# Kernel optimization log

Hardware: AMD Instinct MI355X
Metric: run time of the kernel (lower is better)

The kernel has to match this reference:

```python
import jax, jax.numpy as jnp
import numpy as np
import math

D_MODEL = 1024
N_HEADS = 16
HEAD_DIM = D_MODEL // N_HEADS  # 64
KV_DIM = 4 * HEAD_DIM          # 256
THETA = 10000.0
B, T = 2, 2048


def setup_inputs() -> dict:
    key = jax.random.key(0)
    ks = jax.random.split(key, 14)
    s = lambda k, *sh: jax.random.normal(k, sh, dtype=jnp.float32) * 0.02
    inp = {
        "x": jax.random.normal(ks[0], (B, T, D_MODEL), dtype=jnp.float32),
        "mask": jnp.tril(jnp.ones((T, T), dtype=jnp.int32))[None, None],  # causal [1,1,T,T]
        "Wq": s(ks[1], D_MODEL, D_MODEL), "bq": jnp.zeros((D_MODEL,), jnp.float32),
        "Wkv": s(ks[2], D_MODEL, KV_DIM), "bkv": jnp.zeros((KV_DIM,), jnp.float32),
        "Wk": s(ks[3], KV_DIM, D_MODEL), "bk": jnp.zeros((D_MODEL,), jnp.float32),
        "Wv": s(ks[4], KV_DIM, D_MODEL), "bv": jnp.zeros((D_MODEL,), jnp.float32),
        "Wo": s(ks[5], D_MODEL, D_MODEL), "bo": jnp.zeros((D_MODEL,), jnp.float32),
        "Wkr": s(ks[6], HEAD_DIM, HEAD_DIM),  # decoupled k_rope linear, no bias
    }
    return inp


def _rotate_half(x):
    x1, x2 = jnp.split(x, 2, axis=-1)
    return jnp.concatenate((-x2, x1), axis=-1)


def reference(x, mask, Wq, bq, Wkv, bkv, Wk, bk, Wv, bv, Wo, bo, Wkr):
    Bq, Tq, C = x.shape
    kv = x @ Wkv + bkv                                # [B,T,KV_DIM]
    k = (kv @ Wk + bk).reshape(Bq, Tq, N_HEADS, HEAD_DIM).transpose(0, 2, 1, 3)
    v = (kv @ Wv + bv).reshape(Bq, Tq, N_HEADS, HEAD_DIM).transpose(0, 2, 1, 3)
    q = (x @ Wq + bq).reshape(Bq, Tq, N_HEADS, HEAD_DIM).transpose(0, 2, 1, 3)

    # standard RoPE on q
    inv_freq = 1.0 / (THETA ** (jnp.arange(0, HEAD_DIM, 2, dtype=jnp.float32) / HEAD_DIM))
    t = jnp.arange(Tq, dtype=jnp.float32)
    freqs = t[:, None] * inv_freq[None, :]            # [T, D/2]
    emb = jnp.concatenate((freqs, freqs), axis=-1)    # [T, D]
    q = q * jnp.cos(emb) + _rotate_half(q) * jnp.sin(emb)

    # decoupled position path for k: scale by position index, then linear
    k = (k * t[None, None, :, None]) @ Wkr            # [B,H,T,D]

    attn = jnp.einsum('bhtd,bhsd->bhts', q, k) * (1.0 / math.sqrt(HEAD_DIM))
    attn = jnp.where(mask == 0, -jnp.inf, attn)
    attn = jax.nn.softmax(attn, axis=-1)
    y = jnp.einsum('bhts,bhsd->bhtd', attn, v)
    y = y.transpose(0, 2, 1, 3).reshape(Bq, Tq, C)
    return y @ Wo + bo
```

## Files before the change

kernel.cpp:

```cpp
#include <hip/hip_runtime.h>
#include <hip/hip_bf16.h>
#include <math.h>

typedef __bf16 bf16x8 __attribute__((ext_vector_type(8)));
typedef __bf16 bf16x4 __attribute__((ext_vector_type(4)));
typedef float  f32x4  __attribute__((ext_vector_type(4)));

#define T_SEQ 2048
#define NH    16
#define HD    64
#define DM    1024
#define QSCALE 0.18033688011112043f

__device__ __forceinline__ f32x4 mfma16(bf16x8 a, bf16x8 b, f32x4 c) {
    return __builtin_amdgcn_mfma_f32_16x16x32_bf16(a, b, c, 0, 0, 0);
}

__device__ __forceinline__ void gl2lds(const void* g, void* l) {
    __builtin_amdgcn_global_load_lds(
        (const __attribute__((address_space(1))) void*)g,
        (__attribute__((address_space(3))) void*)l, 16, 0, 0);
}

__device__ __forceinline__ void tsplit_body(const float* __restrict__ in,
                                            __bf16* __restrict__ oh, __bf16* __restrict__ ol,
                                            int K, int N, int n0, int k0, int SPLIT,
                                            float* tile )
{
    const int tid = threadIdx.x;
#pragma unroll
    for (int it = 0; it < 2; ++it) {
        int r = it * 32 + (tid >> 3), c8 = (tid & 7) * 8;
        f32x4 a0 = *(const f32x4*)&in[(size_t)(k0 + r) * N + n0 + c8];
        f32x4 a1 = *(const f32x4*)&in[(size_t)(k0 + r) * N + n0 + c8 + 4];
#pragma unroll
        for (int j = 0; j < 4; ++j) { tile[r * 65 + c8 + j] = a0[j]; tile[r * 65 + c8 + 4 + j] = a1[j]; }
    }
    __syncthreads();
    const int n = tid >> 2, kb = (tid & 3) * 16;
    bf16x8 h0, h1, l0, l1;
#pragma unroll
    for (int j = 0; j < 8; ++j) {
        float v0 = tile[(kb + j) * 65 + n], v1 = tile[(kb + 8 + j) * 65 + n];
        __bf16 hb0 = (__bf16)v0, hb1 = (__bf16)v1;
        h0[j] = hb0; h1[j] = hb1;
        if (SPLIT) { l0[j] = (__bf16)(v0 - (float)hb0); l1[j] = (__bf16)(v1 - (float)hb1); }
    }
    size_t o = (size_t)(n0 + n) * K + k0 + kb;
    *(bf16x8*)&oh[o] = h0; *(bf16x8*)&oh[o + 8] = h1;
    if (SPLIT) { *(bf16x8*)&ol[o] = l0; *(bf16x8*)&ol[o + 8] = l1; }
}

__global__ __launch_bounds__(256)
void prep(const float* __restrict__ x, const float* __restrict__ Wq,
          const float* __restrict__ Wkv, const float* __restrict__ Wv,
          const float* __restrict__ Wo, const float* __restrict__ Wk,
          const float* __restrict__ Wkr, const float* __restrict__ bk,
          __bf16* xh, __bf16* xl, __bf16* Wqt_h, __bf16* Wqt_l,
          __bf16* Wkvt_h, __bf16* Wkvt_l, __bf16* Wvt, __bf16* Wot,
          __bf16* W2th, __bf16* W2tl, float* b2)
{
    __shared__ float tile[64 * 65];
    const int g = blockIdx.x, tid = threadIdx.x;
    if (g < 2048) {
        size_t idx = ((size_t)g * 256 + tid) * 8;
        f32x4 a0 = *(const f32x4*)&x[idx];
        f32x4 a1 = *(const f32x4*)&x[idx + 4];
        bf16x8 h, l;
#pragma unroll
        for (int j = 0; j < 4; ++j) {
            __bf16 h0 = (__bf16)a0[j];
            h[j]     = h0; l[j]     = (__bf16)(a0[j] - (float)h0);
            __bf16 h1 = (__bf16)a1[j];
            h[4 + j] = h1; l[4 + j] = (__bf16)(a1[j] - (float)h1);
        }
        *(bf16x8*)&xh[idx] = h;
        *(bf16x8*)&xl[idx] = l;
    } else if (g < 2304) {
        int i = g - 2048;
        tsplit_body(Wq, Wqt_h, Wqt_l, 1024, 1024, (i & 15) * 64, (i >> 4) * 64, 1, tile);
    } else if (g < 2368) {
        int i = g - 2304;
        tsplit_body(Wkv, Wkvt_h, Wkvt_l, 1024, 256, (i & 3) * 64, (i >> 2) * 64, 1, tile);
    } else if (g < 2432) {
        int i = g - 2368;
        tsplit_body(Wv, Wvt, nullptr, 256, 1024, (i & 15) * 64, (i >> 4) * 64, 0, tile);
    } else if (g < 2688) {
        int i = g - 2432;
        tsplit_body(Wo, Wot, nullptr, 1024, 1024, (i & 15) * 64, (i >> 4) * 64, 0, tile);
    } else {
        int o    = (g - 2688) * 256 + tid;
        int rowk = o >> 10, col = o & 1023;
        int h = col >> 6, d = col & 63;
        float acc = 0.0f;
        if (rowk < 256) {
#pragma unroll 8
            for (int j = 0; j < 64; ++j)
                acc += Wk[(size_t)rowk * DM + h * HD + j] * Wkr[j * HD + d];
            __bf16 hb = (__bf16)acc;
            W2th[(size_t)col * 256 + rowk] = hb;
            W2tl[(size_t)col * 256 + rowk] = (__bf16)(acc - (float)hb);
        } else {
#pragma unroll 8
            for (int j = 0; j < 64; ++j)
                acc += bk[h * HD + j] * Wkr[j * HD + d];
            b2[col] = acc;
        }
    }
}

template <int DUALA, int DUALB, int OUTM, int EPI>
__device__ __forceinline__
void gemm_body(char* smem,
               const __bf16* __restrict__ Ahi, const __bf16* __restrict__ Alo,
               const __bf16* __restrict__ Bhi, const __bf16* __restrict__ Blo,
               const float* __restrict__ bias, void* __restrict__ Cp,
               void* __restrict__ Cp2, int m0, int n0, int N, int K)
{
    const int tid  = threadIdx.x;
    const int w    = tid >> 6;
    const int lane = tid & 63;
    const int l16  = lane & 15;
    const int quad = lane >> 4;
    const int wy   = w >> 1, wx = w & 1;

    f32x4 acc[4][4];
#pragma unroll
    for (int i = 0; i < 4; ++i)
#pragma unroll
        for (int j = 0; j < 4; ++j) acc[i][j] = (f32x4)0.0f;

    auto stage = [&](int k0, int buf) {
        char* bb = smem + buf * 32768;
#pragma unroll
        for (int i = 0; i < 2; ++i) {
            int s = i * 256 + tid, row = s >> 2, c8 = (s & 3) * 8;
            size_t aoff = (size_t)(m0 + row) * K + k0 + c8;
            size_t boff = (size_t)(n0 + row) * K + k0 + c8;
            char*  dst  = bb + (row * 32 + c8) * 2;
            gl2lds(&Ahi[aoff], dst);
            if (DUALA) gl2lds(&Alo[aoff], dst + 8192);
            gl2lds(&Bhi[boff], dst + 16384);
            if (DUALB) gl2lds(&Blo[boff], dst + 24576);
        }
    };

    stage(0, 0);
    const int J = K >> 5;
    for (int j = 0; j < J; ++j) {
        __syncthreads();
        if (j + 1 < J) stage((j + 1) << 5, (j + 1) & 1);

        const __bf16* Ah = (const __bf16*)(smem + (j & 1) * 32768);
        const __bf16* Al = Ah + 4096;
        const __bf16* Bh = Ah + 8192;
        const __bf16* Bl = Ah + 12288;

        bf16x8 bfh[4], bfl[4];
#pragma unroll
        for (int ct = 0; ct < 4; ++ct) {
            bfh[ct] = *(const bf16x8*)&Bh[(wx * 64 + ct * 16 + l16) * 32 + quad * 8];
            if (DUALB) bfl[ct] = *(const bf16x8*)&Bl[(wx * 64 + ct * 16 + l16) * 32 + quad * 8];
        }
#pragma unroll
        for (int mf = 0; mf < 4; ++mf) {
            bf16x8 ah = *(const bf16x8*)&Ah[(wy * 64 + mf * 16 + l16) * 32 + quad * 8];
            bf16x8 al;
            if (DUALA) al = *(const bf16x8*)&Al[(wy * 64 + mf * 16 + l16) * 32 + quad * 8];
#pragma unroll
            for (int ct = 0; ct < 4; ++ct) {
                acc[mf][ct] = mfma16(ah, bfh[ct], acc[mf][ct]);
                if (DUALA) acc[mf][ct] = mfma16(al, bfh[ct], acc[mf][ct]);
                if (DUALB) acc[mf][ct] = mfma16(ah, bfl[ct], acc[mf][ct]);
            }
        }
    }

    float bias_v[4];
#pragma unroll
    for (int ct = 0; ct < 4; ++ct)
        bias_v[ct] = bias ? bias[n0 + wx * 64 + ct * 16 + l16] : 0.0f;

    if (EPI == 1) {
        __bf16* Chi = (__bf16*)Cp;
        __bf16* Clo = (__bf16*)Cp2;
#pragma unroll
        for (int mf = 0; mf < 4; ++mf) {
#pragma unroll
            for (int r = 0; r < 4; ++r) {
                int   m = m0 + wy * 64 + mf * 16 + quad * 4 + r;
                float t = (float)(m & (T_SEQ - 1));
#pragma unroll
                for (int ct = 0; ct < 2; ++ct) {
                    int   d   = ct * 16 + l16;
                    float inv = powf(10000.0f, -(float)d * (1.0f / 32.0f));
                    float sv, cv;
                    sincosf(t * inv, &sv, &cv);
                    float lo = acc[mf][ct][r]     + bias_v[ct];
                    float hi = acc[mf][ct + 2][r] + bias_v[ct + 2];
                    float v0 = (lo * cv - hi * sv) * QSCALE;
                    float v1 = (hi * cv + lo * sv) * QSCALE;
                    size_t i0 = (size_t)m * N + n0 + wx * 64 + d;
                    size_t i1 = i0 + 32;
                    __bf16 h0 = (__bf16)v0, h1 = (__bf16)v1;
                    Chi[i0] = h0; Clo[i0] = (__bf16)(v0 - (float)h0);
                    Chi[i1] = h1; Clo[i1] = (__bf16)(v1 - (float)h1);
                }
            }
        }
    } else if (EPI == 3) {
        __syncthreads();
        __bf16* vt = (__bf16*)(smem + w * 9216);
#pragma unroll
        for (int mf = 0; mf < 4; ++mf)
#pragma unroll
            for (int ct = 0; ct < 4; ++ct)
#pragma unroll
                for (int r = 0; r < 4; ++r)
                    vt[(ct * 16 + l16) * 72 + mf * 16 + quad * 4 + r] =
                        (__bf16)(acc[mf][ct][r] + bias_v[ct]);
        const int bb   = m0 >> 11;
        const int head = (n0 + wx * 64) >> 6;
        const int bh   = bb * 16 + head;
        __bf16* out    = (__bf16*)Cp;
        size_t  gbase  = ((size_t)(bh * 64 + lane)) * T_SEQ + (m0 & (T_SEQ - 1)) + wy * 64;
#pragma unroll
        for (int j8 = 0; j8 < 8; ++j8)
            *(bf16x8*)&out[gbase + j8 * 8] = *(const bf16x8*)&vt[lane * 72 + j8 * 8];
    } else {
#pragma unroll
        for (int mf = 0; mf < 4; ++mf) {
#pragma unroll
            for (int r = 0; r < 4; ++r) {
                int   m     = m0 + wy * 64 + mf * 16 + quad * 4 + r;
                float scale = (EPI == 2) ? (float)(m & (T_SEQ - 1)) : 1.0f;
#pragma unroll
                for (int ct = 0; ct < 4; ++ct) {
                    float  v   = (acc[mf][ct][r] + bias_v[ct]) * scale;
                    size_t idx = (size_t)m * N + n0 + wx * 64 + ct * 16 + l16;
                    if (OUTM == 1)      ((float*)Cp)[idx]  = v;
                    else if (OUTM == 0) ((__bf16*)Cp)[idx] = (__bf16)v;
                    else {
                        __bf16 hb = (__bf16)v;
                        ((__bf16*)Cp)[idx]  = hb;
                        ((__bf16*)Cp2)[idx] = (__bf16)(v - (float)hb);
                    }
                }
            }
        }
    }
}

__global__ __launch_bounds__(256)
void gemm_qkv(const __bf16* xh, const __bf16* xl,
              const __bf16* Wqt_h, const __bf16* Wqt_l, const float* bq,
              __bf16* qhi, __bf16* qlo,
              const __bf16* Wkvt_h, const __bf16* Wkvt_l, const float* bkv,
              __bf16* kvhi, __bf16* kvlo)
{
    __shared__ __attribute__((aligned(16))) char smem[65536];
    const int m0 = blockIdx.y * 128;
    if (blockIdx.x < 2)
        gemm_body<1, 1, 2, 0>(smem, xh, xl, Wkvt_h, Wkvt_l, bkv, kvhi, kvlo,
                              m0, blockIdx.x * 128, 256, 1024);
    else
        gemm_body<1, 1, 2, 1>(smem, xh, xl, Wqt_h, Wqt_l, bq, qhi, qlo,
                              m0, (blockIdx.x - 2) * 128, 1024, 1024);
}

__global__ __launch_bounds__(256)
void gemm_kv2(const __bf16* kvhi, const __bf16* kvlo,
              const __bf16* W2th, const __bf16* W2tl, const float* b2,
              __bf16* khi, __bf16* klo,
              const __bf16* Wvt, const float* bv, __bf16* vtg)
{
    __shared__ __attribute__((aligned(16))) char smem[65536];
    const int m0 = blockIdx.y * 128;
    if (blockIdx.x < 8)
        gemm_body<1, 1, 2, 2>(smem, kvhi, kvlo, W2th, W2tl, b2, khi, klo,
                              m0, blockIdx.x * 128, 1024, 256);
    else
        gemm_body<1, 0, 0, 3>(smem, kvhi, kvlo, Wvt, Wvt, bv, vtg, nullptr,
                              m0, (blockIdx.x - 8) * 128, 1024, 256);
}

__global__ __launch_bounds__(256)
void gemm_o(const __bf16* ybb, const __bf16* Wot, const float* bo, float* out)
{
    __shared__ __attribute__((aligned(16))) char smem[65536];
    gemm_body<0, 0, 1, 0>(smem, ybb, ybb, Wot, Wot, bo, out, nullptr,
                          blockIdx.y * 128, blockIdx.x * 128, 1024, 1024);
}

#define KSP 72
#define PSP 72
__global__ __launch_bounds__(256, 2)
void attn_v5(const __bf16* __restrict__ qhi, const __bf16* __restrict__ qlo,
             const __bf16* __restrict__ khi, const __bf16* __restrict__ klo,
             const __bf16* __restrict__ vtg, __bf16* __restrict__ yb)
{
    __shared__ __attribute__((aligned(16))) __bf16 Kh2[2][64 * KSP];
    __shared__ __attribute__((aligned(16))) __bf16 Kl2[2][64 * KSP];
    __shared__ __attribute__((aligned(16))) __bf16 Vt2[2][64 * KSP];
    __shared__ __attribute__((aligned(16))) __bf16 Pw[4][2][16 * PSP];

    const int tid  = threadIdx.x;
    const int w    = tid >> 6;
    const int lane = tid & 63;
    const int l16  = lane & 15;
    const int quad = lane >> 4;

    const int g  = blockIdx.x;
    const int bh = g & 31, a = g >> 5;
    const int tile = (a < 8) ? (15 - 2 * a) : (2 * (a - 8));
    const int b = bh >> 4, h = bh & 15;
    const int q0 = tile * 128;

    bf16x8 qh[2][2], ql[2][2];
#pragma unroll
    for (int f = 0; f < 2; ++f) {
        const int    qrow = q0 + 64 * f + 16 * w + l16;
        const size_t qoff = (size_t)(b * T_SEQ + qrow) * DM + h * HD;
#pragma unroll
        for (int s = 0; s < 2; ++s) {
            qh[f][s] = *(const bf16x8*)&qhi[qoff + s * 32 + quad * 8];
            ql[f][s] = *(const bf16x8*)&qlo[qoff + s * 32 + quad * 8];
        }
    }

    f32x4 o[2][4];
#pragma unroll
    for (int f = 0; f < 2; ++f)
#pragma unroll
        for (int i = 0; i < 4; ++i) o[f][i] = (f32x4)0.0f;
    float m_i[2] = {-1e30f, -1e30f}, l_i[2] = {0.f, 0.f};

    const int srow = tid >> 3, sc8 = (tid & 7) * 8;
    bf16x8 kr[2], lr[2], vr[2];

#pragma unroll
    for (int it = 0; it < 2; ++it) {
        int    r  = it * 32 + srow;
        size_t gk = (size_t)(b * T_SEQ + r) * DM + h * HD + sc8;
        kr[it] = *(const bf16x8*)&khi[gk];
        lr[it] = *(const bf16x8*)&klo[gk];
        vr[it] = *(const bf16x8*)&vtg[(size_t)(bh * HD + r) * T_SEQ + sc8];
    }
#pragma unroll
    for (int it = 0; it < 2; ++it) {
        int r = it * 32 + srow;
        *(bf16x8*)&Kh2[0][r * KSP + sc8] = kr[it];
        *(bf16x8*)&Kl2[0][r * KSP + sc8] = lr[it];
        *(bf16x8*)&Vt2[0][r * KSP + sc8] = vr[it];
    }

    const int jmax = q0 + 64;
    for (int j0 = 0; j0 <= jmax; j0 += 64) {
        const int  cur  = (j0 >> 6) & 1;
        const bool act0 = (j0 <= q0);
        const bool pre  = (j0 + 64 <= jmax);
        __syncthreads();

        if (pre) {
#pragma unroll
            for (int it = 0; it < 2; ++it) {
                int    r  = it * 32 + srow;
                size_t gk = (size_t)(b * T_SEQ + j0 + 64 + r) * DM + h * HD + sc8;
                kr[it] = *(const bf16x8*)&khi[gk];
                lr[it] = *(const bf16x8*)&klo[gk];
                vr[it] = *(const bf16x8*)&vtg[(size_t)(bh * HD + r) * T_SEQ + j0 + 64 + sc8];
            }
        }

        const __bf16* Kh = Kh2[cur];
        const __bf16* Kl = Kl2[cur];
        const __bf16* Vt = Vt2[cur];

        f32x4 sa[2][4];
#pragma unroll
        for (int f = 0; f < 2; ++f)
#pragma unroll
            for (int i = 0; i < 4; ++i) sa[f][i] = (f32x4)0.0f;
#pragma unroll
        for (int s = 0; s < 2; ++s) {
#pragma unroll
            for (int kc = 0; kc < 4; ++kc) {
                bf16x8 kh = *(const bf16x8*)&Kh[(kc * 16 + l16) * KSP + s * 32 + quad * 8];
                bf16x8 kv = *(const bf16x8*)&Kl[(kc * 16 + l16) * KSP + s * 32 + quad * 8];
                sa[1][kc] = mfma16(kh, qh[1][s], sa[1][kc]);
                sa[1][kc] = mfma16(kv, qh[1][s], sa[1][kc]);
                sa[1][kc] = mfma16(kh, ql[1][s], sa[1][kc]);
                if (act0) {
                    sa[0][kc] = mfma16(kh, qh[0][s], sa[0][kc]);
                    sa[0][kc] = mfma16(kv, qh[0][s], sa[0][kc]);
                    sa[0][kc] = mfma16(kh, ql[0][s], sa[0][kc]);
                }
            }
        }

#pragma unroll
        for (int f = 0; f < 2; ++f) {
            if (f == 0 && !act0) continue;
            const int  qrow = q0 + 64 * f + 16 * w + l16;
            const bool need = (j0 + 63 > q0 + 64 * f + 16 * w);
            if (need) {
#pragma unroll
                for (int kc = 0; kc < 4; ++kc)
#pragma unroll
                    for (int r = 0; r < 4; ++r)
                        if (j0 + kc * 16 + quad * 4 + r > qrow) sa[f][kc][r] = -1e30f;
            }
            float mx = -1e30f;
#pragma unroll
            for (int kc = 0; kc < 4; ++kc)
#pragma unroll
                for (int r = 0; r < 4; ++r) mx = fmaxf(mx, sa[f][kc][r]);
            mx = fmaxf(mx, __shfl_xor(mx, 16));
            mx = fmaxf(mx, __shfl_xor(mx, 32));
            float mn    = fmaxf(fmaxf(m_i[f], mx), -1e20f);
            float alpha = exp2f(m_i[f] - mn);
            m_i[f] = mn;
            float rs = 0.f;
            __bf16* pw = &Pw[w][f][0];
#pragma unroll
            for (int kc = 0; kc < 4; ++kc) {
                float p0 = exp2f(sa[f][kc][0] - mn);
                float p1 = exp2f(sa[f][kc][1] - mn);
                float p2 = exp2f(sa[f][kc][2] - mn);
                float p3 = exp2f(sa[f][kc][3] - mn);
                rs += (p0 + p1) + (p2 + p3);
                bf16x4 pk = { (__bf16)p0, (__bf16)p1, (__bf16)p2, (__bf16)p3 };
                *(bf16x4*)&pw[l16 * PSP + kc * 16 + quad * 4] = pk;
            }
            rs += __shfl_xor(rs, 16);
            rs += __shfl_xor(rs, 32);
            l_i[f] = l_i[f] * alpha + rs;
#pragma unroll
            for (int dc = 0; dc < 4; ++dc) o[f][dc] *= alpha;
        }

#pragma unroll
        for (int s = 0; s < 2; ++s) {
            bf16x8 pb1 = *(const bf16x8*)&Pw[w][1][l16 * PSP + s * 32 + quad * 8];
            bf16x8 pb0;
            if (act0) pb0 = *(const bf16x8*)&Pw[w][0][l16 * PSP + s * 32 + quad * 8];
#pragma unroll
            for (int dc = 0; dc < 4; ++dc) {
                bf16x8 va = *(const bf16x8*)&Vt[(dc * 16 + l16) * KSP + s * 32 + quad * 8];
                o[1][dc] = mfma16(va, pb1, o[1][dc]);
                if (act0) o[0][dc] = mfma16(va, pb0, o[0][dc]);
            }
        }

        if (pre) {
            __bf16* nKh = Kh2[cur ^ 1];
            __bf16* nKl = Kl2[cur ^ 1];
            __bf16* nVt = Vt2[cur ^ 1];
#pragma unroll
            for (int it = 0; it < 2; ++it) {
                int r = it * 32 + srow;
                *(bf16x8*)&nKh[r * KSP + sc8] = kr[it];
                *(bf16x8*)&nKl[r * KSP + sc8] = lr[it];
                *(bf16x8*)&nVt[r * KSP + sc8] = vr[it];
            }
        }
    }

#pragma unroll
    for (int f = 0; f < 2; ++f) {
        float   invl = 1.0f / l_i[f];
        __bf16* pw   = &Pw[w][f][0];
#pragma unroll
        for (int dc = 0; dc < 4; ++dc) {
            bf16x4 ov = { (__bf16)(o[f][dc][0] * invl), (__bf16)(o[f][dc][1] * invl),
                          (__bf16)(o[f][dc][2] * invl), (__bf16)(o[f][dc][3] * invl) };
            *(bf16x4*)&pw[l16 * PSP + dc * 16 + quad * 4] = ov;
        }
        const int qrl  = lane >> 2;
        const int dch  = (lane & 3) * 16;
        const int qrow = q0 + 64 * f + 16 * w + qrl;
        const __bf16* src = &pw[qrl * PSP + dch];
        __bf16*       dst = &yb[(size_t)(b * T_SEQ + qrow) * DM + h * HD + dch];
        *(bf16x8*)dst       = *(const bf16x8*)src;
        *(bf16x8*)(dst + 8) = *(const bf16x8*)(src + 8);
    }
}

extern "C" void kernel_launch(void* const* d_in, const int* in_sizes, int n_in,
                              void* d_out, int out_size, void* d_ws, size_t ws_size,
                              hipStream_t stream)
{
    (void)in_sizes; (void)n_in; (void)out_size; (void)ws_size;

    const float* x   = (const float*)d_in[0];
    const float* Wq  = (const float*)d_in[2];
    const float* bq  = (const float*)d_in[3];
    const float* Wkv = (const float*)d_in[4];
    const float* bkv = (const float*)d_in[5];
    const float* Wk  = (const float*)d_in[6];
    const float* bk  = (const float*)d_in[7];
    const float* Wv  = (const float*)d_in[8];
    const float* bv  = (const float*)d_in[9];
    const float* Wo  = (const float*)d_in[10];
    const float* bo  = (const float*)d_in[11];
    const float* Wkr = (const float*)d_in[12];

    const int    BT = 2 * T_SEQ;
    const size_t MB = 1024 * 1024;
    char* base = (char*)d_ws;

    __bf16* xhi    = (__bf16*)(base +  0 * MB);
    __bf16* xlo    = (__bf16*)(base +  8 * MB);
    __bf16* qhi    = (__bf16*)(base + 16 * MB);
    __bf16* qlo    = (__bf16*)(base + 24 * MB);
    __bf16* Wqt_h  = (__bf16*)(base + 32 * MB);
    __bf16* Wqt_l  = (__bf16*)(base + 34 * MB);
    __bf16* Wkvt_h = (__bf16*)(base + 36 * MB);
    __bf16* Wkvt_l = (__bf16*)(base + 37 * MB);
    __bf16* kvhi   = (__bf16*)(base + 38 * MB);
    __bf16* kvlo   = (__bf16*)(base + 40 * MB);
    __bf16* W2t_h  = (__bf16*)(base + 42 * MB);
    __bf16* W2t_l  = (__bf16*)(base + 42 * MB + 512 * 1024);
    __bf16* Wvt    = (__bf16*)(base + 43 * MB);
    __bf16* Wot    = (__bf16*)(base + 43 * MB + 512 * 1024);
    float*  b2     = (float*) (base + 45 * MB + 512 * 1024);
    __bf16* vtg    = (__bf16*)(base +  8 * MB);
    __bf16* ybb    = (__bf16*)(base +  0 * MB);
    __bf16* khi    = (__bf16*)d_out;
    __bf16* klo    = (__bf16*)d_out + (size_t)BT * DM;

    dim3 blk(256);
    prep<<<3716, blk, 0, stream>>>(x, Wq, Wkv, Wv, Wo, Wk, Wkr, bk,
                                   xhi, xlo, Wqt_h, Wqt_l, Wkvt_h, Wkvt_l,
                                   Wvt, Wot, W2t_h, W2t_l, b2);
    gemm_qkv<<<dim3(10, 32), blk, 0, stream>>>(xhi, xlo, Wqt_h, Wqt_l, bq, qhi, qlo,
                                               Wkvt_h, Wkvt_l, bkv, kvhi, kvlo);
    gemm_kv2<<<dim3(16, 32), blk, 0, stream>>>(kvhi, kvlo, W2t_h, W2t_l, b2,
                                               khi, klo, Wvt, bv, vtg);
    attn_v5<<<512, blk, 0, stream>>>(qhi, qlo, khi, klo, vtg, ybb);
    gemm_o<<<dim3(8, 32), blk, 0, stream>>>(ybb, Wot, bo, (float*)d_out);
}
```

Baseline: 279.8 us.

## Load K hi/lo fragments directly from global memory instead of LDS staging

The attention kernel stops staging K (hi and lo bf16 parts) through double-buffered shared memory. Each wave now reads its MFMA K fragments straight from global memory, and only V stays in LDS. This cuts LDS usage and the launch bound is raised to 3 blocks per SM for higher occupancy. In exchange, all four waves issue redundant global and L2 reads of the same K tile, and those loads are no longer prefetched a tile ahead, so their latency sits in the critical path before the MFMAs.

```diff
diff --git a/kernel.cpp b/kernel.cpp
--- a/kernel.cpp
+++ b/kernel.cpp
@@ -294,13 +294,11 @@
 
 #define KSP 72
 #define PSP 72
-__global__ __launch_bounds__(256, 2)
-void attn_v5(const __bf16* __restrict__ qhi, const __bf16* __restrict__ qlo,
+__global__ __launch_bounds__(256, 3)
+void attn_v7(const __bf16* __restrict__ qhi, const __bf16* __restrict__ qlo,
              const __bf16* __restrict__ khi, const __bf16* __restrict__ klo,
              const __bf16* __restrict__ vtg, __bf16* __restrict__ yb)
 {
-    __shared__ __attribute__((aligned(16))) __bf16 Kh2[2][64 * KSP];
-    __shared__ __attribute__((aligned(16))) __bf16 Kl2[2][64 * KSP];
     __shared__ __attribute__((aligned(16))) __bf16 Vt2[2][64 * KSP];
     __shared__ __attribute__((aligned(16))) __bf16 Pw[4][2][16 * PSP];
 
@@ -336,23 +334,20 @@
     float m_i[2] = {-1e30f, -1e30f}, l_i[2] = {0.f, 0.f};
 
     const int srow = tid >> 3, sc8 = (tid & 7) * 8;
-    bf16x8 kr[2], lr[2], vr[2];
-
-#pragma unroll
-    for (int it = 0; it < 2; ++it) {
-        int    r  = it * 32 + srow;
-        size_t gk = (size_t)(b * T_SEQ + r) * DM + h * HD + sc8;
-        kr[it] = *(const bf16x8*)&khi[gk];
-        lr[it] = *(const bf16x8*)&klo[gk];
-        vr[it] = *(const bf16x8*)&vtg[(size_t)(bh * HD + r) * T_SEQ + sc8];
-    }
+    bf16x8 vr[2];
+
 #pragma unroll
     for (int it = 0; it < 2; ++it) {
         int r = it * 32 + srow;
-        *(bf16x8*)&Kh2[0][r * KSP + sc8] = kr[it];
-        *(bf16x8*)&Kl2[0][r * KSP + sc8] = lr[it];
+        vr[it] = *(const bf16x8*)&vtg[(size_t)(bh * HD + r) * T_SEQ + sc8];
+    }
+#pragma unroll
+    for (int it = 0; it < 2; ++it) {
+        int r = it * 32 + srow;
         *(bf16x8*)&Vt2[0][r * KSP + sc8] = vr[it];
     }
+
+    const size_t kbase0 = (size_t)(b * T_SEQ + l16) * DM + h * HD + quad * 8;
 
     const int jmax = q0 + 64;
     for (int j0 = 0; j0 <= jmax; j0 += 64) {
@@ -364,18 +359,11 @@
         if (pre) {
 #pragma unroll
             for (int it = 0; it < 2; ++it) {
-                int    r  = it * 32 + srow;
-                size_t gk = (size_t)(b * T_SEQ + j0 + 64 + r) * DM + h * HD + sc8;
-                kr[it] = *(const bf16x8*)&khi[gk];
-                lr[it] = *(const bf16x8*)&klo[gk];
+                int r = it * 32 + srow;
                 vr[it] = *(const bf16x8*)&vtg[(size_t)(bh * HD + r) * T_SEQ + j0 + 64 + sc8];
             }
         }
 
-        const __bf16* Kh = Kh2[cur];
-        const __bf16* Kl = Kl2[cur];
-        const __bf16* Vt = Vt2[cur];
-
         f32x4 sa[2][4];
 #pragma unroll
         for (int f = 0; f < 2; ++f)
@@ -383,17 +371,22 @@
             for (int i = 0; i < 4; ++i) sa[f][i] = (f32x4)0.0f;
 #pragma unroll
         for (int s = 0; s < 2; ++s) {
+            bf16x8 kh[4], kl[4];
 #pragma unroll
             for (int kc = 0; kc < 4; ++kc) {
-                bf16x8 kh = *(const bf16x8*)&Kh[(kc * 16 + l16) * KSP + s * 32 + quad * 8];
-                bf16x8 kv = *(const bf16x8*)&Kl[(kc * 16 + l16) * KSP + s * 32 + quad * 8];
-                sa[1][kc] = mfma16(kh, qh[1][s], sa[1][kc]);
-                sa[1][kc] = mfma16(kv, qh[1][s], sa[1][kc]);
-                sa[1][kc] = mfma16(kh, ql[1][s], sa[1][kc]);
+                size_t gk = kbase0 + (size_t)(j0 + kc * 16) * DM + s * 32;
+                kh[kc] = *(const bf16x8*)&khi[gk];
+                kl[kc] = *(const bf16x8*)&klo[gk];
+            }
+#pragma unroll
+            for (int kc = 0; kc < 4; ++kc) {
+                sa[1][kc] = mfma16(kh[kc], qh[1][s], sa[1][kc]);
+                sa[1][kc] = mfma16(kl[kc], qh[1][s], sa[1][kc]);
+                sa[1][kc] = mfma16(kh[kc], ql[1][s], sa[1][kc]);
                 if (act0) {
-                    sa[0][kc] = mfma16(kh, qh[0][s], sa[0][kc]);
-                    sa[0][kc] = mfma16(kv, qh[0][s], sa[0][kc]);
-                    sa[0][kc] = mfma16(kh, ql[0][s], sa[0][kc]);
+                    sa[0][kc] = mfma16(kh[kc], qh[0][s], sa[0][kc]);
+                    sa[0][kc] = mfma16(kl[kc], qh[0][s], sa[0][kc]);
+                    sa[0][kc] = mfma16(kh[kc], ql[0][s], sa[0][kc]);
                 }
             }
         }
@@ -439,6 +432,7 @@
             for (int dc = 0; dc < 4; ++dc) o[f][dc] *= alpha;
         }
 
+        const __bf16* Vt = Vt2[cur];
 #pragma unroll
         for (int s = 0; s < 2; ++s) {
             bf16x8 pb1 = *(const bf16x8*)&Pw[w][1][l16 * PSP + s * 32 + quad * 8];
@@ -453,14 +447,10 @@
         }
 
         if (pre) {
-            __bf16* nKh = Kh2[cur ^ 1];
-            __bf16* nKl = Kl2[cur ^ 1];
             __bf16* nVt = Vt2[cur ^ 1];
 #pragma unroll
             for (int it = 0; it < 2; ++it) {
                 int r = it * 32 + srow;
-                *(bf16x8*)&nKh[r * KSP + sc8] = kr[it];
-                *(bf16x8*)&nKl[r * KSP + sc8] = lr[it];
                 *(bf16x8*)&nVt[r * KSP + sc8] = vr[it];
             }
         }
@@ -537,6 +527,6 @@
                                                Wkvt_h, Wkvt_l, bkv, kvhi, kvlo);
     gemm_kv2<<<dim3(16, 32), blk, 0, stream>>>(kvhi, kvlo, W2t_h, W2t_l, b2,
                                                khi, klo, Wvt, bv, vtg);
-    attn_v5<<<512, blk, 0, stream>>>(qhi, qlo, khi, klo, vtg, ybb);
+    attn_v7<<<512, blk, 0, stream>>>(qhi, qlo, khi, klo, vtg, ybb);
     gemm_o<<<dim3(8, 32), blk, 0, stream>>>(ybb, Wot, bo, (float*)d_out);
 }
```

New measurement: 313.9 us. 1.12x slower.
